# Kernel optimization log

Measured on AMD Instinct MI355X. Metric: run time of the kernel, lower is better.

## Reference

```python
import jax, jax.numpy as jnp
import numpy as np

B, S, NB = 8, 512, 23
INIT, E, R, T = 512, 256, 3, 2
NEG = -9e8

def _gru(x, h, wih, whh, bih, bhh):
    gi = x @ wih.T + bih
    gh = h @ whh.T + bhh
    ir, iz, inn = jnp.split(gi, 3, axis=-1)
    hr, hz, hn = jnp.split(gh, 3, axis=-1)
    r = jax.nn.sigmoid(ir + hr)
    z = jax.nn.sigmoid(iz + hz)
    n = jnp.tanh(inn + r * hn)
    return (1.0 - z) * n + z * h

def setup_inputs():
    key = jax.random.key(0)
    ks = jax.random.split(key, 30)
    def lin(k, o, i):
        return jax.random.normal(k, (o, i), jnp.float32) * 0.02
    def vec(k, n):
        return jax.random.normal(k, (n,), jnp.float32) * 0.02
    inp = {}
    inp["amino_list"] = jax.random.normal(ks[0], (B, S, INIT), jnp.float32)
    inp["amino_mask"] = (jax.random.uniform(ks[1], (B, S)) < 0.9).astype(jnp.float32)
    inp["emb_W"] = lin(ks[2], E, INIT); inp["emb_b"] = vec(ks[3], E)
    inp["nb_W"] = lin(ks[4], E, INIT); inp["nb_b"] = vec(ks[5], E)
    inp["align_W"] = jax.random.normal(ks[6], (R, 1, 2 * E), jnp.float32) * 0.02
    inp["align_b"] = jax.random.normal(ks[7], (R, 1), jnp.float32) * 0.02
    inp["attend_W"] = jax.random.normal(ks[8], (R, E, E), jnp.float32) * 0.02
    inp["attend_b"] = jax.random.normal(ks[9], (R, E), jnp.float32) * 0.02
    inp["gru_wih"] = jax.random.normal(ks[10], (R, 3 * E, E), jnp.float32) * 0.02
    inp["gru_whh"] = jax.random.normal(ks[11], (R, 3 * E, E), jnp.float32) * 0.02
    inp["gru_bih"] = jax.random.normal(ks[12], (R, 3 * E), jnp.float32) * 0.02
    inp["gru_bhh"] = jax.random.normal(ks[13], (R, 3 * E), jnp.float32) * 0.02
    inp["seq_align_W"] = lin(ks[14], 1, 2 * E); inp["seq_align_b"] = vec(ks[15], 1)
    inp["seq_attend_W"] = lin(ks[16], E, E); inp["seq_attend_b"] = vec(ks[17], E)
    inp["seq_gru_wih"] = lin(ks[18], 3 * E, E); inp["seq_gru_bih"] = vec(ks[19], 3 * E)
    inp["seq_gru_whh"] = lin(ks[20], 3 * E, E); inp["seq_gru_bhh"] = vec(ks[21], 3 * E)
    inp["amino_degree_list"] = jax.random.randint(ks[22], (B, S, NB), -1, S)
    return inp

def reference(amino_list, amino_mask, emb_W, emb_b, nb_W, nb_b, align_W, align_b,
              attend_W, attend_b, gru_wih, gru_whh, gru_bih, gru_bhh,
              seq_align_W, seq_align_b, seq_attend_W, seq_attend_b,
              seq_gru_wih, seq_gru_whh, seq_gru_bih, seq_gru_bhh, amino_degree_list):
    idx = amino_degree_list
    lrelu = jax.nn.leaky_relu
    # per-batch neighbor gather: (S,D),(S,NB) -> (S,NB,D); index -1 wraps (masked out below)
    gather = jax.vmap(lambda f, i: f[i])
    feat = lrelu(amino_list @ emb_W.T + emb_b)               # (B,S,E)
    nfeat = lrelu(gather(amino_list, idx) @ nb_W.T + nb_b)   # (B,S,NB,E)
    attend_mask = (idx != -1).astype(feat.dtype)             # (B,S,NB)
    smask = jnp.where(idx == -1, NEG, 0.0).astype(feat.dtype)

    def attn(d, center, nbr):
        # align Linear on concat([center, nbr]) split into two matvecs (same math, no concat)
        aW = align_W[d, 0]
        score = lrelu(jnp.einsum('bse,e->bs', center, aW[:E])[:, :, None]
                      + jnp.einsum('bsne,e->bsn', nbr, aW[E:]) + align_b[d, 0])
        w = jax.nn.softmax(score + smask, axis=-1) * attend_mask   # softmax over neighbor axis
        nt = nbr @ attend_W[d].T + attend_b[d]
        return jax.nn.elu(jnp.einsum('bsn,bsne->bse', w, nt))

    h = _gru(attn(0, feat, nfeat).reshape(-1, E), feat.reshape(-1, E),
             gru_wih[0], gru_whh[0], gru_bih[0], gru_bhh[0])
    act = jax.nn.relu(h.reshape(B, S, E))
    for d in range(1, R):
        ctx = attn(d, act, gather(act, idx))
        h = _gru(ctx.reshape(-1, E), h, gru_wih[d], gru_whh[d], gru_bih[d], gru_bhh[d])
        act = jax.nn.relu(h.reshape(B, S, E))

    seq_feature = jnp.sum(act * amino_mask[:, :, None], axis=1)  # (B,E)
    act_mol = jax.nn.relu(seq_feature)                           # fixed across T (as in torch)
    seq_smask = jnp.where(amino_mask == 0, NEG, 0.0)
    saW = seq_align_W[0]
    act_seq = act_mol
    for _ in range(T):
        score = lrelu((act_mol @ saW[:E])[:, None]
                      + jnp.einsum('bse,e->bs', act, saW[E:]) + seq_align_b[0])
        w = jax.nn.softmax(score + seq_smask, axis=-1) * amino_mask  # softmax over seq axis
        tf = act @ seq_attend_W.T + seq_attend_b
        seq_ctx = jax.nn.elu(jnp.einsum('bs,bse->be', w, tf))
        seq_feature = _gru(seq_ctx, seq_feature, seq_gru_wih, seq_gru_whh, seq_gru_bih, seq_gru_bhh)
        act_seq = jax.nn.relu(seq_feature)
    return (act_seq, act)
```

## Files before the change

### kernel.cpp

```cpp
#include <hip/hip_runtime.h>
#include <math.h>


#define BSZ   8
#define SEQ   512
#define NBR   23
#define EMB   256
#define INITD 512
#define BS    (BSZ*SEQ)
#define G3    (3*EMB)
#define NEGV  -9e8f

typedef __attribute__((ext_vector_type(8))) short short8;
typedef __attribute__((ext_vector_type(4))) float f32x4;

__device__ __forceinline__ float lrelu(float x){ return x > 0.f ? x : 0.01f*x; }
__device__ __forceinline__ float elu1 (float x){ return x > 0.f ? x : (expf(x)-1.f); }
__device__ __forceinline__ float sigm (float x){ return 1.f/(1.f+expf(-x)); }
__device__ __forceinline__ float bf2f(ushort u){
    union { unsigned int i; float f; } v; v.i = ((unsigned int)u) << 16; return v.f;
}
__device__ __forceinline__ ushort f2bf(float f){
    union { float f; unsigned int i; } v; v.f = f;
    unsigned int u = v.i;
    return (ushort)((u + 0x7FFFu + ((u >> 16) & 1u)) >> 16);
}
__device__ __forceinline__ unsigned pk2(float a, float b){
    return (unsigned)f2bf(a) | ((unsigned)f2bf(b) << 16);
}
__device__ __forceinline__ void unpack8(uint4 v, float* o) {
    o[0]=bf2f((ushort)(v.x&0xffff)); o[1]=bf2f((ushort)(v.x>>16));
    o[2]=bf2f((ushort)(v.y&0xffff)); o[3]=bf2f((ushort)(v.y>>16));
    o[4]=bf2f((ushort)(v.z&0xffff)); o[5]=bf2f((ushort)(v.z>>16));
    o[6]=bf2f((ushort)(v.w&0xffff)); o[7]=bf2f((ushort)(v.w>>16));
}

__device__ __forceinline__ void gload_lds16(const void* g, void* l) {
    __builtin_amdgcn_global_load_lds(
        (const __attribute__((address_space(1))) unsigned int*)g,
        (__attribute__((address_space(3))) unsigned int*)l,
        16, 0, 0);
}

__global__ __launch_bounds__(256) void convert9_kernel(
    const float* s0, ushort* d0, int n0,
    const float* s1, ushort* d1, int n1,
    const float* s2, ushort* d2, int n2,
    const float* s3, ushort* d3, int n3,
    const float* s4, ushort* d4, int n4,
    const float* s5, ushort* d5, int n5,
    const float* s6, ushort* d6, int n6,
    const float* s7, ushort* d7, int n7,
    const float* s8, ushort* d8, int n8)
{
    const float* srcs[9] = {s0,s1,s2,s3,s4,s5,s6,s7,s8};
    ushort* dsts[9] = {d0,d1,d2,d3,d4,d5,d6,d7,d8};
    int ns[9] = {n0,n1,n2,n3,n4,n5,n6,n7,n8};
    int seg = blockIdx.y;
    const float* s = srcs[seg]; ushort* d = dsts[seg]; int n = ns[seg];
    size_t i = ((size_t)blockIdx.x * 256 + threadIdx.x) * 8;
    size_t stride = (size_t)gridDim.x * 256 * 8;
    for (; i < (size_t)n; i += stride) {
        float4 a = *reinterpret_cast<const float4*>(s + i);
        float4 b = *reinterpret_cast<const float4*>(s + i + 4);
        uint4 o;
        o.x = pk2(a.x, a.y); o.y = pk2(a.z, a.w);
        o.z = pk2(b.x, b.y); o.w = pk2(b.z, b.w);
        *reinterpret_cast<uint4*>(d + i) = o;
    }
}

struct GemmLds64 { ushort A[2][128][64]; ushort B[2][64][64]; };

template<int ACT>
__device__ __forceinline__ void gemm64_dev(
    const ushort* __restrict__ A, const ushort* __restrict__ W,
    const float* __restrict__ bias,
    float* __restrict__ C, ushort* __restrict__ Cbf,
    int N, int K, int bx, int by, GemmLds64& L)
{
    const int tid = threadIdx.x;
    const int m0 = bx * 128, n0 = by * 64;
    const int wv = tid >> 6, lane = tid & 63;
    const int fr = lane & 15, grp = lane >> 4;
    const int kc = K >> 3;
    const int mh = wv & 1, nh = wv >> 1;
    const int lrow = lane >> 3;
    const int csrc = (lane & 7) ^ lrow;

    f32x4 acc[4][2];
    #pragma unroll
    for (int i = 0; i < 4; ++i)
        #pragma unroll
        for (int n = 0; n < 2; ++n) acc[i][n] = (f32x4){0.f,0.f,0.f,0.f};

    auto stage = [&](int c, int k0) {
        const int kch = (k0 >> 3) + csrc;
        #pragma unroll
        for (int i = 0; i < 4; ++i) {
            const int s = (wv << 2) + i;
            gload_lds16(A + ((size_t)(m0 + (s << 3) + lrow) * kc + kch) * 8,
                        &L.A[c][s << 3][0]);
        }
        #pragma unroll
        for (int i = 0; i < 2; ++i) {
            const int s = (wv << 1) + i;
            gload_lds16(W + ((size_t)(n0 + (s << 3) + lrow) * kc + kch) * 8,
                        &L.B[c][s << 3][0]);
        }
    };
    auto compute = [&](int c) {
        #pragma unroll
        for (int ks = 0; ks < 2; ++ks) {
            short8 af[4];
            #pragma unroll
            for (int i = 0; i < 4; ++i) {
                const int ar = (mh << 6) + (i << 4) + fr;
                af[i] = *reinterpret_cast<const short8*>(
                    &L.A[c][ar][(((ks << 2) + grp) ^ (ar & 7)) << 3]);
            }
            #pragma unroll
            for (int n = 0; n < 2; ++n) {
                const int br = (nh << 5) + (n << 4) + fr;
                short8 bv = *reinterpret_cast<const short8*>(
                    &L.B[c][br][(((ks << 2) + grp) ^ (br & 7)) << 3]);
                #pragma unroll
                for (int i = 0; i < 4; ++i)
                    acc[i][n] = __builtin_amdgcn_mfma_f32_16x16x32_bf16(
                        af[i], bv, acc[i][n], 0, 0, 0);
            }
        }
    };

    const int KT = K >> 6;
    stage(0, 0);
    __syncthreads();
    int cur = 0;
    for (int kt = 1; kt < KT; ++kt) {
        stage(cur ^ 1, kt << 6);
        compute(cur);
        __syncthreads();
        cur ^= 1;
    }
    compute(cur);

    #pragma unroll
    for (int i = 0; i < 4; ++i) {
        const int mrow = m0 + (mh << 6) + (i << 4) + (grp << 2);
        #pragma unroll
        for (int n = 0; n < 2; ++n) {
            const int col = n0 + (nh << 5) + (n << 4) + fr;
            const float bv = bias[col];
            #pragma unroll
            for (int j = 0; j < 4; ++j) {
                float t = acc[i][n][j] + bv;
                if (ACT == 1) t = lrelu(t);
                size_t off = (size_t)(mrow + j) * N + col;
                if (C)   C[off] = t;
                if (Cbf) Cbf[off] = f2bf(t);
            }
        }
    }
}

__global__ __launch_bounds__(256) void featnbase_kernel(
    const ushort* __restrict__ aminobf,
    const ushort* __restrict__ embWbf, const float* __restrict__ embB,
    float* __restrict__ feat, ushort* __restrict__ featbf,
    const ushort* __restrict__ nbWbf, const float* __restrict__ nbB,
    float* __restrict__ nbase, ushort* __restrict__ nbasebf)
{
    __shared__ GemmLds64 L;
    int blk = blockIdx.x;
    if (blk < 128)
        gemm64_dev<1>(aminobf, embWbf, embB, feat, featbf, EMB, INITD, blk & 31, blk >> 5, L);
    else {
        blk -= 128;
        gemm64_dev<1>(aminobf, nbWbf, nbB, nbase, nbasebf, EMB, INITD, blk & 31, blk >> 5, L);
    }
}

__global__ __launch_bounds__(256) void dot2_kernel(
    const float* __restrict__ center, const float* __restrict__ nbrbase,
    const float* __restrict__ alignWd,
    float* __restrict__ cdot, float* __restrict__ ndot)
{
    const int lane = threadIdx.x & 63;
    const int wv   = threadIdx.x >> 6;
    const int e    = lane << 2;
    const int rb   = blockIdx.x * 32 + wv * 8;
    float4 w0 = *reinterpret_cast<const float4*>(&alignWd[e]);
    float4 w1 = *reinterpret_cast<const float4*>(&alignWd[EMB + e]);
    #pragma unroll
    for (int i = 0; i < 8; ++i) {
        const int r = rb + i;
        float4 xc = *reinterpret_cast<const float4*>(&center[(size_t)r*EMB + e]);
        float4 xn = *reinterpret_cast<const float4*>(&nbrbase[(size_t)r*EMB + e]);
        float ac = xc.x*w0.x + xc.y*w0.y + xc.z*w0.z + xc.w*w0.w;
        float an = xn.x*w1.x + xn.y*w1.y + xn.z*w1.z + xn.w*w1.w;
        #pragma unroll
        for (int off = 32; off; off >>= 1) {
            ac += __shfl_xor(ac, off, 64);
            an += __shfl_xor(an, off, 64);
        }
        if (lane == 0) { cdot[r] = ac; ndot[r] = an; }
    }
}

struct GALds { ushort ctxpre[16][256]; ushort ctx[16][256]; float wsum_s[16]; };

__global__ __launch_bounds__(512) void gatherattend_kernel(
    const float* __restrict__ cdot, const float* __restrict__ ndot,
    const int* __restrict__ idx, const ushort* __restrict__ nbr,
    const float* __restrict__ alignBd,
    const ushort* __restrict__ attWd, const float* __restrict__ attBd,
    ushort* __restrict__ ctxbf)
{
    __shared__ GALds L;
    const int tid = threadIdx.x;
    const int r0 = blockIdx.x * 16;

    {
        const int row16 = tid >> 5, sub = tid & 31;
        const int r = r0 + row16, b = r >> 9;
        float sc = -3e38f, vm = 0.f; int rn = 0;
        if (sub < NBR) {
            int j = idx[(size_t)r*NBR + sub];
            int valid = (j >= 0);
            int jj = valid ? j : j + SEQ;
            rn = b*SEQ + jj;
            vm = (float)valid;
            sc = lrelu(cdot[r] + ndot[rn] + alignBd[0]) + (valid ? 0.f : NEGV);
        }
        float m = sc;
        #pragma unroll
        for (int off = 16; off; off >>= 1) m = fmaxf(m, __shfl_xor(m, off, 32));
        float ev = (sub < NBR) ? expf(sc - m) : 0.f;
        float s = ev;
        #pragma unroll
        for (int off = 16; off; off >>= 1) s += __shfl_xor(s, off, 32);
        float wgt = ev * vm / s;
        float ws = wgt;
        #pragma unroll
        for (int off = 16; off; off >>= 1) ws += __shfl_xor(ws, off, 32);
        float a8[8] = {};
        const int e0 = sub << 3;
        #pragma unroll
        for (int n = 0; n < NBR; ++n) {
            float wn = __shfl(wgt, n, 32);
            int   rr = __shfl(rn, n, 32);
            uint4 v = *reinterpret_cast<const uint4*>(&nbr[(size_t)rr*EMB + e0]);
            float x[8]; unpack8(v, x);
            #pragma unroll
            for (int i = 0; i < 8; ++i) a8[i] += wn * x[i];
        }
        uint4 o;
        o.x = pk2(a8[0],a8[1]); o.y = pk2(a8[2],a8[3]);
        o.z = pk2(a8[4],a8[5]); o.w = pk2(a8[6],a8[7]);
        *reinterpret_cast<uint4*>(&L.ctxpre[row16][(sub ^ (row16&7)) << 3]) = o;
        if (sub == 0) L.wsum_s[row16] = ws;
    }
    __syncthreads();

    const int wv = tid >> 6, lane = tid & 63;
    const int fr = lane & 15, grp = lane >> 4;
    {
        f32x4 acc[2] = {(f32x4){0,0,0,0},(f32x4){0,0,0,0}};
        #pragma unroll
        for (int kt = 0; kt < 8; ++kt) {
            short8 af = *reinterpret_cast<const short8*>(
                &L.ctxpre[fr][((((kt<<2)+grp) ^ (fr&7)) << 3)]);
            #pragma unroll
            for (int f = 0; f < 2; ++f) {
                const int col = (wv<<5) + (f<<4) + fr;
                short8 bv = *reinterpret_cast<const short8*>(
                    &attWd[(size_t)col*EMB + (kt<<5) + (grp<<3)]);
                acc[f] = __builtin_amdgcn_mfma_f32_16x16x32_bf16(af, bv, acc[f], 0, 0, 0);
            }
        }
        #pragma unroll
        for (int f = 0; f < 2; ++f) {
            const int col = (wv<<5) + (f<<4) + fr;
            const float bb = attBd[col];
            #pragma unroll
            for (int j = 0; j < 4; ++j) {
                const int row = (grp<<2) + j;
                L.ctx[row][col] = f2bf(elu1(acc[f][j] + L.wsum_s[row]*bb));
            }
        }
    }
    __syncthreads();
    {
        const int row = tid >> 5, c = tid & 31;
        uint4 v = *reinterpret_cast<const uint4*>(&L.ctx[row][c << 3]);
        *reinterpret_cast<uint4*>(&ctxbf[(size_t)(r0+row)*EMB + (c << 3)]) = v;
    }
}

__global__ __launch_bounds__(256) void gigh_kernel(
    const ushort* __restrict__ ctxbf, const ushort* __restrict__ gwihd,
    const float* __restrict__ gbihd, ushort* __restrict__ gibf,
    const ushort* __restrict__ hprevbf, const ushort* __restrict__ gwhhd,
    const float* __restrict__ gbhhd, ushort* __restrict__ ghbf)
{
    __shared__ GemmLds64 L;
    int blk = blockIdx.x;
    if (blk < 384)
        gemm64_dev<0>(ctxbf, gwihd, gbihd, nullptr, gibf, G3, EMB, blk & 31, blk >> 5, L);
    else {
        blk -= 384;
        gemm64_dev<0>(hprevbf, gwhhd, gbhhd, nullptr, ghbf, G3, EMB, blk & 31, blk >> 5, L);
    }
}

template<int LAST>
__global__ __launch_bounds__(512) void grudot_kernel(
    const ushort* __restrict__ gibf, const ushort* __restrict__ ghbf,
    const float* __restrict__ hprev, const float* __restrict__ nextW,
    float* __restrict__ hout, ushort* __restrict__ hbf,
    float* __restrict__ actout, ushort* __restrict__ actbf,
    float* __restrict__ cdotO, float* __restrict__ ndotO)
{
    const int tid = threadIdx.x;
    const int row = tid >> 5, sub = tid & 31;
    const int e0 = sub << 3;
    const size_t r = (size_t)blockIdx.x * 16 + row;
    const size_t gb = r*G3;
    uint4 giA = *reinterpret_cast<const uint4*>(&gibf[gb + e0]);
    uint4 giB = *reinterpret_cast<const uint4*>(&gibf[gb + 256 + e0]);
    uint4 giC = *reinterpret_cast<const uint4*>(&gibf[gb + 512 + e0]);
    uint4 ghA = *reinterpret_cast<const uint4*>(&ghbf[gb + e0]);
    uint4 ghB = *reinterpret_cast<const uint4*>(&ghbf[gb + 256 + e0]);
    uint4 ghC = *reinterpret_cast<const uint4*>(&ghbf[gb + 512 + e0]);
    float4 hp0 = *reinterpret_cast<const float4*>(&hprev[r*EMB + e0]);
    float4 hp1 = *reinterpret_cast<const float4*>(&hprev[r*EMB + e0 + 4]);
    float ir_[8], iz_[8], in_[8], hr_[8], hz_[8], hn_[8];
    unpack8(giA, ir_); unpack8(giB, iz_); unpack8(giC, in_);
    unpack8(ghA, hr_); unpack8(ghB, hz_); unpack8(ghC, hn_);
    const float hp_[8] = {hp0.x,hp0.y,hp0.z,hp0.w,hp1.x,hp1.y,hp1.z,hp1.w};
    float hv8[8], av8[8];
    #pragma unroll
    for (int i = 0; i < 8; ++i) {
        float rg = sigm(ir_[i] + hr_[i]);
        float z  = sigm(iz_[i] + hz_[i]);
        float n  = tanhf(in_[i] + rg*hn_[i]);
        hv8[i] = (1.f - z)*n + z*hp_[i];
        av8[i] = fmaxf(hv8[i], 0.f);
    }
    *reinterpret_cast<float4*>(&hout[r*EMB + e0])       = make_float4(hv8[0],hv8[1],hv8[2],hv8[3]);
    *reinterpret_cast<float4*>(&hout[r*EMB + e0 + 4])   = make_float4(hv8[4],hv8[5],hv8[6],hv8[7]);
    *reinterpret_cast<float4*>(&actout[r*EMB + e0])     = make_float4(av8[0],av8[1],av8[2],av8[3]);
    *reinterpret_cast<float4*>(&actout[r*EMB + e0 + 4]) = make_float4(av8[4],av8[5],av8[6],av8[7]);
    uint4 hb, ab;
    hb.x = pk2(hv8[0],hv8[1]); hb.y = pk2(hv8[2],hv8[3]);
    hb.z = pk2(hv8[4],hv8[5]); hb.w = pk2(hv8[6],hv8[7]);
    ab.x = pk2(av8[0],av8[1]); ab.y = pk2(av8[2],av8[3]);
    ab.z = pk2(av8[4],av8[5]); ab.w = pk2(av8[6],av8[7]);
    *reinterpret_cast<uint4*>(&hbf[r*EMB + e0])   = hb;
    *reinterpret_cast<uint4*>(&actbf[r*EMB + e0]) = ab;
    float pc = 0.f, pn = 0.f;
    float4 w1a = *reinterpret_cast<const float4*>(&nextW[EMB + e0]);
    float4 w1b = *reinterpret_cast<const float4*>(&nextW[EMB + e0 + 4]);
    pn = av8[0]*w1a.x + av8[1]*w1a.y + av8[2]*w1a.z + av8[3]*w1a.w
       + av8[4]*w1b.x + av8[5]*w1b.y + av8[6]*w1b.z + av8[7]*w1b.w;
    if (!LAST) {
        float4 w0a = *reinterpret_cast<const float4*>(&nextW[e0]);
        float4 w0b = *reinterpret_cast<const float4*>(&nextW[e0 + 4]);
        pc = av8[0]*w0a.x + av8[1]*w0a.y + av8[2]*w0a.z + av8[3]*w0a.w
           + av8[4]*w0b.x + av8[5]*w0b.y + av8[6]*w0b.z + av8[7]*w0b.w;
    }
    #pragma unroll
    for (int off = 16; off; off >>= 1) {
        pn += __shfl_xor(pn, off, 32);
        if (!LAST) pc += __shfl_xor(pc, off, 32);
    }
    if (sub == 0) {
        if (!LAST) cdotO[r] = pc;
        ndotO[r] = pn;
    }
}

__global__ __launch_bounds__(256) void seqpre_kernel(
    const ushort* __restrict__ actbf, const ushort* __restrict__ satWbf,
    const float* __restrict__ satB, float* __restrict__ tf,
    const float* __restrict__ act, const float* __restrict__ mask,
    const float* __restrict__ saW,
    float* __restrict__ seqfeat, float* __restrict__ cmol)
{
    __shared__ GemmLds64 L;
    int blk = blockIdx.x;
    if (blk < 128) {
        gemm64_dev<0>(actbf, satWbf, satB, tf, nullptr, EMB, EMB, blk & 31, blk >> 5, L);
    } else {
        const int b = blk - 128;
        const int e = threadIdx.x;
        float acc = 0.f;
        for (int s = 0; s < SEQ; ++s)
            acc += act[((size_t)b*SEQ + s)*EMB + e] * mask[b*SEQ + s];
        seqfeat[b*EMB + e] = acc;
        float* red = reinterpret_cast<float*>(&L);
        red[e] = fmaxf(acc, 0.f) * saW[e];
        __syncthreads();
        for (int off = 128; off; off >>= 1) {
            if (e < off) red[e] += red[e + off];
            __syncthreads();
        }
        if (e == 0) cmol[b] = red[0];
    }
}

__global__ __launch_bounds__(256) void seqpv2_kernel(
    const float* __restrict__ ad, const float* __restrict__ mask,
    const float* __restrict__ saB, const float* __restrict__ cmol,
    const float* __restrict__ tf, float* __restrict__ partial)
{
    const int st = blockIdx.x, b = blockIdx.y;
    const int tid = threadIdx.x;
    __shared__ float w_s[SEQ];
    __shared__ float red[256];
    float mk0 = mask[b*SEQ + tid], mk1 = mask[b*SEQ + 256 + tid];
    float cb = cmol[b], bb = saB[0];
    float s0 = lrelu(cb + ad[b*SEQ + tid] + bb)       + (mk0 == 0.f ? NEGV : 0.f);
    float s1 = lrelu(cb + ad[b*SEQ + 256 + tid] + bb) + (mk1 == 0.f ? NEGV : 0.f);
    red[tid] = fmaxf(s0, s1); __syncthreads();
    for (int off = 128; off; off >>= 1) {
        if (tid < off) red[tid] = fmaxf(red[tid], red[tid + off]);
        __syncthreads();
    }
    float m = red[0]; __syncthreads();
    float e0 = expf(s0 - m), e1 = expf(s1 - m);
    red[tid] = e0 + e1; __syncthreads();
    for (int off = 128; off; off >>= 1) {
        if (tid < off) red[tid] += red[tid + off];
        __syncthreads();
    }
    float inv = 1.f / red[0];
    w_s[tid]       = e0 * inv * mk0;
    w_s[tid + 256] = e1 * inv * mk1;
    __syncthreads();
    float acc = 0.f;
    const int s0i = st * 32;
    #pragma unroll 4
    for (int s = s0i; s < s0i + 32; ++s)
        acc += w_s[s] * tf[((size_t)b*SEQ + s)*EMB + tid];
    partial[((size_t)b*16 + st)*EMB + tid] = acc;
}

template<int T0>
__global__ __launch_bounds__(512) void seqstep_kernel(
    const float* __restrict__ partial, const float* __restrict__ sfin,
    const ushort* __restrict__ sgwihbf, const float* __restrict__ sgbih,
    const ushort* __restrict__ sgwhhbf, const float* __restrict__ sgbhh,
    float* __restrict__ sgi, float* __restrict__ sfout,
    float* __restrict__ actseq)
{
    const int b = blockIdx.x >> 2, q = blockIdx.x & 3;
    const int tid = threadIdx.x, lane = tid & 63, wv = tid >> 6;
    __shared__ float xs[EMB];
    __shared__ float hs[EMB];
    __shared__ float gis[192], ghs[192];
    if (tid < EMB) {
        hs[tid] = sfin[b*EMB + tid];
        if (T0) {
            float a = 0.f;
            #pragma unroll
            for (int st = 0; st < 16; ++st)
                a += partial[((size_t)b*16 + st)*EMB + tid];
            xs[tid] = elu1(a);
        }
    }
    if (!T0) {
        for (int l = tid; l < 192; l += 512) {
            int g = (l >> 6)*EMB + (q << 6) + (l & 63);
            gis[l] = sgi[b*G3 + g];
        }
    }
    __syncthreads();
    const int nrows = T0 ? 384 : 192;
    const int rpw = nrows >> 3;
    for (int i = 0; i < rpw; ++i) {
        const int l = wv * rpw + i;
        const int iswih = T0 && (l < 192);
        const int ll = (T0 && l >= 192) ? l - 192 : l;
        const int g = (ll >> 6)*EMB + (q << 6) + (ll & 63);
        const ushort* Wm = iswih ? sgwihbf : sgwhhbf;
        ushort4 w4 = *reinterpret_cast<const ushort4*>(&Wm[(size_t)g*EMB + (lane << 2)]);
        float4 x4 = *reinterpret_cast<const float4*>(iswih ? &xs[lane << 2] : &hs[lane << 2]);
        float d = bf2f(w4.x)*x4.x + bf2f(w4.y)*x4.y + bf2f(w4.z)*x4.z + bf2f(w4.w)*x4.w;
        #pragma unroll
        for (int off = 32; off; off >>= 1) d += __shfl_xor(d, off, 64);
        if (lane == 0) {
            if (iswih) {
                d += sgbih[g];
                gis[ll] = d;
                sgi[b*G3 + g] = d;
            } else {
                ghs[ll] = d + sgbhh[g];
            }
        }
    }
    __syncthreads();
    if (tid < 64) {
        const int e = (q << 6) + tid;
        float rg = sigm(gis[tid]       + ghs[tid]);
        float z  = sigm(gis[64 + tid]  + ghs[64 + tid]);
        float n  = tanhf(gis[128 + tid] + rg*ghs[128 + tid]);
        float hv = (1.f - z)*n + z*hs[e];
        sfout[b*EMB + e]  = hv;
        actseq[b*EMB + e] = fmaxf(hv, 0.f);
    }
}

extern "C" void kernel_launch(void* const* d_in, const int* in_sizes, int n_in,
                              void* d_out, int out_size, void* d_ws, size_t ws_size,
                              hipStream_t stream) {
    (void)in_sizes; (void)n_in; (void)out_size; (void)ws_size;
    const float* amino  = (const float*)d_in[0];
    const float* mask   = (const float*)d_in[1];
    const float* embW   = (const float*)d_in[2];
    const float* embB   = (const float*)d_in[3];
    const float* nbW    = (const float*)d_in[4];
    const float* nbB    = (const float*)d_in[5];
    const float* alignW = (const float*)d_in[6];
    const float* alignB = (const float*)d_in[7];
    const float* attW   = (const float*)d_in[8];
    const float* attB   = (const float*)d_in[9];
    const float* gwih   = (const float*)d_in[10];
    const float* gwhh   = (const float*)d_in[11];
    const float* gbih   = (const float*)d_in[12];
    const float* gbhh   = (const float*)d_in[13];
    const float* saW    = (const float*)d_in[14];
    const float* saB    = (const float*)d_in[15];
    const float* satW   = (const float*)d_in[16];
    const float* satB   = (const float*)d_in[17];
    const float* sgwih  = (const float*)d_in[18];
    const float* sgbih  = (const float*)d_in[19];
    const float* sgwhh  = (const float*)d_in[20];
    const float* sgbhh  = (const float*)d_in[21];
    const int*   idx    = (const int*)d_in[22];

    char* cur = (char*)d_ws;
    auto alloc = [&](size_t bytes) -> char* {
        char* p = cur; cur += (bytes + 255) & ~(size_t)255; return p;
    };
    float* feat    = (float*)alloc((size_t)BS*EMB*4);
    float* nbase   = (float*)alloc((size_t)BS*EMB*4);
    float* h       = (float*)alloc((size_t)BS*EMB*4);
    float* tf      = (float*)alloc((size_t)BS*EMB*4);
    float* cdot    = (float*)alloc(BS*4);
    float* ndot    = (float*)alloc(BS*4);
    float* seqfeat = (float*)alloc(BSZ*EMB*4);
    float* sf2     = (float*)alloc(BSZ*EMB*4);
    float* cmol    = (float*)alloc(64*4);
    float* sgi     = (float*)alloc(BSZ*G3*4);
    float* partial = (float*)alloc((size_t)BSZ*16*EMB*4);
    ushort* aminobf  = (ushort*)alloc((size_t)BS*INITD*2);
    ushort* featbf   = (ushort*)alloc((size_t)BS*EMB*2);
    ushort* nbasebf  = (ushort*)alloc((size_t)BS*EMB*2);
    ushort* actbf    = (ushort*)alloc((size_t)BS*EMB*2);
    ushort* hbf      = (ushort*)alloc((size_t)BS*EMB*2);
    ushort* ctxbf    = (ushort*)alloc((size_t)BS*EMB*2);
    ushort* gibf     = (ushort*)alloc((size_t)BS*G3*2);
    ushort* ghbf     = (ushort*)alloc((size_t)BS*G3*2);
    ushort* embWbf   = (ushort*)alloc((size_t)EMB*INITD*2);
    ushort* nbWbf    = (ushort*)alloc((size_t)EMB*INITD*2);
    ushort* attWbf   = (ushort*)alloc((size_t)3*EMB*EMB*2);
    ushort* gwihbf   = (ushort*)alloc((size_t)3*G3*EMB*2);
    ushort* gwhhbf   = (ushort*)alloc((size_t)3*G3*EMB*2);
    ushort* satWbf   = (ushort*)alloc((size_t)EMB*EMB*2);
    ushort* sgwihbf  = (ushort*)alloc((size_t)G3*EMB*2);
    ushort* sgwhhbf  = (ushort*)alloc((size_t)G3*EMB*2);

    float* out    = (float*)d_out;
    float* actseq = out;
    float* act    = out + BSZ*EMB;

    convert9_kernel<<<dim3(1024, 9), 256, 0, stream>>>(
        amino, aminobf, BS*INITD,
        embW,  embWbf,  EMB*INITD,
        nbW,   nbWbf,   EMB*INITD,
        attW,  attWbf,  3*EMB*EMB,
        gwih,  gwihbf,  3*G3*EMB,
        gwhh,  gwhhbf,  3*G3*EMB,
        satW,  satWbf,  EMB*EMB,
        sgwih, sgwihbf, G3*EMB,
        sgwhh, sgwhhbf, G3*EMB);

    featnbase_kernel<<<256, 256, 0, stream>>>(
        aminobf, embWbf, embB, feat, featbf, nbWbf, nbB, nbase, nbasebf);

    dot2_kernel<<<128, 256, 0, stream>>>(feat, nbase, alignW, cdot, ndot);

    for (int d = 0; d < 3; ++d) {
        const ushort* nbrbf   = (d == 0) ? nbasebf : actbf;
        const float*  hprev   = (d == 0) ? feat    : h;
        const ushort* hprevbf = (d == 0) ? featbf  : hbf;
        gatherattend_kernel<<<BS/16, 512, 0, stream>>>(
            cdot, ndot, idx, nbrbf, alignB + d,
            attWbf + (size_t)d*EMB*EMB, attB + d*EMB, ctxbf);
        gigh_kernel<<<768, 256, 0, stream>>>(
            ctxbf, gwihbf + (size_t)d*G3*EMB, gbih + d*G3, gibf,
            hprevbf, gwhhbf + (size_t)d*G3*EMB, gbhh + d*G3, ghbf);
        if (d < 2) {
            grudot_kernel<0><<<BS/16, 512, 0, stream>>>(
                gibf, ghbf, hprev, alignW + (d+1)*2*EMB,
                h, hbf, act, actbf, cdot, ndot);
        } else {
            grudot_kernel<1><<<BS/16, 512, 0, stream>>>(
                gibf, ghbf, hprev, saW,
                h, hbf, act, actbf, cdot, ndot);
        }
    }

    seqpre_kernel<<<136, 256, 0, stream>>>(
        actbf, satWbf, satB, tf, act, mask, saW, seqfeat, cmol);
    seqpv2_kernel<<<dim3(16, BSZ), 256, 0, stream>>>(ndot, mask, saB, cmol, tf, partial);
    seqstep_kernel<1><<<32, 512, 0, stream>>>(
        partial, seqfeat, sgwihbf, sgbih, sgwhhbf, sgbhh, sgi, sf2, actseq);
    seqstep_kernel<0><<<32, 512, 0, stream>>>(
        partial, sf2, sgwihbf, sgbih, sgwhhbf, sgbhh, sgi, seqfeat, actseq);
}
```

Measured before the change: 186.6 us.

## Fuse sequence pooling into GRU epilogue and merge sequence readout kernels

Replaces the per-segment convert kernel with a flat grid-stride converter that also zeroes the pooled sequence-feature buffer. The last GRU epilogue now does the masked sum over sequence positions in shared memory and atomically adds into seqfeat, so the serial per-batch loop in seqpre is removed. The softmax, weighted pooling and first GRU step are merged into one kernel, and a lighter second-step kernel computes only the hidden-state GEMV. The fp32 h buffer is dropped in favour of reading the bf16 copy of the previous hidden state, which adds rounding error, and the atomic pooling makes the summation order nondeterministic.

```diff
diff --git a/kernel.cpp b/kernel.cpp
--- a/kernel.cpp
+++ b/kernel.cpp
@@ -42,25 +42,37 @@
         16, 0, 0);
 }
 
-__global__ __launch_bounds__(256) void convert9_kernel(
-    const float* s0, ushort* d0, int n0,
-    const float* s1, ushort* d1, int n1,
-    const float* s2, ushort* d2, int n2,
-    const float* s3, ushort* d3, int n3,
-    const float* s4, ushort* d4, int n4,
-    const float* s5, ushort* d5, int n5,
-    const float* s6, ushort* d6, int n6,
-    const float* s7, ushort* d7, int n7,
-    const float* s8, ushort* d8, int n8)
-{
-    const float* srcs[9] = {s0,s1,s2,s3,s4,s5,s6,s7,s8};
-    ushort* dsts[9] = {d0,d1,d2,d3,d4,d5,d6,d7,d8};
-    int ns[9] = {n0,n1,n2,n3,n4,n5,n6,n7,n8};
-    int seg = blockIdx.y;
-    const float* s = srcs[seg]; ushort* d = dsts[seg]; int n = ns[seg];
-    size_t i = ((size_t)blockIdx.x * 256 + threadIdx.x) * 8;
-    size_t stride = (size_t)gridDim.x * 256 * 8;
-    for (; i < (size_t)n; i += stride) {
+__global__ __launch_bounds__(256) void convert_flat(
+    const float* __restrict__ amino, ushort* __restrict__ aminobf,
+    const float* __restrict__ embW,  ushort* __restrict__ embWbf,
+    const float* __restrict__ nbW,   ushort* __restrict__ nbWbf,
+    const float* __restrict__ attW,  ushort* __restrict__ attWbf,
+    const float* __restrict__ gwih,  ushort* __restrict__ gwihbf,
+    const float* __restrict__ gwhh,  ushort* __restrict__ gwhhbf,
+    const float* __restrict__ satW,  ushort* __restrict__ satWbf,
+    const float* __restrict__ sgwih, ushort* __restrict__ sgwihbf,
+    const float* __restrict__ sgwhh, ushort* __restrict__ sgwhhbf,
+    float* __restrict__ seqfeatZ)
+{
+    const unsigned stride = gridDim.x * 256;
+    for (unsigned u = blockIdx.x*256 + threadIdx.x; u < 524544u; u += stride) {
+        const float* s; ushort* d; unsigned lu;
+        if      (u < 262144u) { s=amino; d=aminobf; lu=u; }
+        else if (u < 278528u) { s=embW;  d=embWbf;  lu=u-262144u; }
+        else if (u < 294912u) { s=nbW;   d=nbWbf;   lu=u-278528u; }
+        else if (u < 319488u) { s=attW;  d=attWbf;  lu=u-294912u; }
+        else if (u < 393216u) { s=gwih;  d=gwihbf;  lu=u-319488u; }
+        else if (u < 466944u) { s=gwhh;  d=gwhhbf;  lu=u-393216u; }
+        else if (u < 475136u) { s=satW;  d=satWbf;  lu=u-466944u; }
+        else if (u < 499712u) { s=sgwih; d=sgwihbf; lu=u-475136u; }
+        else if (u < 524288u) { s=sgwhh; d=sgwhhbf; lu=u-499712u; }
+        else {
+            unsigned i = (u - 524288u) * 8;
+            *reinterpret_cast<float4*>(&seqfeatZ[i])     = make_float4(0,0,0,0);
+            *reinterpret_cast<float4*>(&seqfeatZ[i + 4]) = make_float4(0,0,0,0);
+            continue;
+        }
+        size_t i = (size_t)lu * 8;
         float4 a = *reinterpret_cast<const float4*>(s + i);
         float4 b = *reinterpret_cast<const float4*>(s + i + 4);
         uint4 o;
@@ -316,11 +328,14 @@
 template<int LAST>
 __global__ __launch_bounds__(512) void grudot_kernel(
     const ushort* __restrict__ gibf, const ushort* __restrict__ ghbf,
-    const float* __restrict__ hprev, const float* __restrict__ nextW,
-    float* __restrict__ hout, ushort* __restrict__ hbf,
-    float* __restrict__ actout, ushort* __restrict__ actbf,
-    float* __restrict__ cdotO, float* __restrict__ ndotO)
-{
+    const ushort* __restrict__ hprevbf, const float* __restrict__ nextW,
+    const float* __restrict__ mask,
+    ushort* __restrict__ hbf, float* __restrict__ actout,
+    ushort* __restrict__ actbf,
+    float* __restrict__ cdotO, float* __restrict__ ndotO,
+    float* __restrict__ seqfeatA)
+{
+    __shared__ float sred[16][256];
     const int tid = threadIdx.x;
     const int row = tid >> 5, sub = tid & 31;
     const int e0 = sub << 3;
@@ -332,12 +347,11 @@
     uint4 ghA = *reinterpret_cast<const uint4*>(&ghbf[gb + e0]);
     uint4 ghB = *reinterpret_cast<const uint4*>(&ghbf[gb + 256 + e0]);
     uint4 ghC = *reinterpret_cast<const uint4*>(&ghbf[gb + 512 + e0]);
-    float4 hp0 = *reinterpret_cast<const float4*>(&hprev[r*EMB + e0]);
-    float4 hp1 = *reinterpret_cast<const float4*>(&hprev[r*EMB + e0 + 4]);
-    float ir_[8], iz_[8], in_[8], hr_[8], hz_[8], hn_[8];
+    uint4 hpv = *reinterpret_cast<const uint4*>(&hprevbf[r*EMB + e0]);
+    float ir_[8], iz_[8], in_[8], hr_[8], hz_[8], hn_[8], hp_[8];
     unpack8(giA, ir_); unpack8(giB, iz_); unpack8(giC, in_);
     unpack8(ghA, hr_); unpack8(ghB, hz_); unpack8(ghC, hn_);
-    const float hp_[8] = {hp0.x,hp0.y,hp0.z,hp0.w,hp1.x,hp1.y,hp1.z,hp1.w};
+    unpack8(hpv, hp_);
     float hv8[8], av8[8];
     #pragma unroll
     for (int i = 0; i < 8; ++i) {
@@ -347,10 +361,10 @@
         hv8[i] = (1.f - z)*n + z*hp_[i];
         av8[i] = fmaxf(hv8[i], 0.f);
     }
-    *reinterpret_cast<float4*>(&hout[r*EMB + e0])       = make_float4(hv8[0],hv8[1],hv8[2],hv8[3]);
-    *reinterpret_cast<float4*>(&hout[r*EMB + e0 + 4])   = make_float4(hv8[4],hv8[5],hv8[6],hv8[7]);
-    *reinterpret_cast<float4*>(&actout[r*EMB + e0])     = make_float4(av8[0],av8[1],av8[2],av8[3]);
-    *reinterpret_cast<float4*>(&actout[r*EMB + e0 + 4]) = make_float4(av8[4],av8[5],av8[6],av8[7]);
+    if (LAST) {
+        *reinterpret_cast<float4*>(&actout[r*EMB + e0])     = make_float4(av8[0],av8[1],av8[2],av8[3]);
+        *reinterpret_cast<float4*>(&actout[r*EMB + e0 + 4]) = make_float4(av8[4],av8[5],av8[6],av8[7]);
+    }
     uint4 hb, ab;
     hb.x = pk2(hv8[0],hv8[1]); hb.y = pk2(hv8[2],hv8[3]);
     hb.z = pk2(hv8[4],hv8[5]); hb.w = pk2(hv8[6],hv8[7]);
@@ -378,77 +392,33 @@
         if (!LAST) cdotO[r] = pc;
         ndotO[r] = pn;
     }
+    if (LAST) {
+        const float mk = mask[r];
+        #pragma unroll
+        for (int i = 0; i < 8; ++i) sred[row][e0 + i] = av8[i] * mk;
+        __syncthreads();
+        if (tid < 256) {
+            float s = 0.f;
+            #pragma unroll
+            for (int rr = 0; rr < 16; ++rr) s += sred[rr][tid];
+            atomicAdd(&seqfeatA[(blockIdx.x >> 5)*EMB + tid], s);
+        }
+    }
 }
 
 __global__ __launch_bounds__(256) void seqpre_kernel(
     const ushort* __restrict__ actbf, const ushort* __restrict__ satWbf,
-    const float* __restrict__ satB, float* __restrict__ tf,
-    const float* __restrict__ act, const float* __restrict__ mask,
-    const float* __restrict__ saW,
-    float* __restrict__ seqfeat, float* __restrict__ cmol)
+    const float* __restrict__ satB, float* __restrict__ tf)
 {
     __shared__ GemmLds64 L;
-    int blk = blockIdx.x;
-    if (blk < 128) {
-        gemm64_dev<0>(actbf, satWbf, satB, tf, nullptr, EMB, EMB, blk & 31, blk >> 5, L);
-    } else {
-        const int b = blk - 128;
-        const int e = threadIdx.x;
-        float acc = 0.f;
-        for (int s = 0; s < SEQ; ++s)
-            acc += act[((size_t)b*SEQ + s)*EMB + e] * mask[b*SEQ + s];
-        seqfeat[b*EMB + e] = acc;
-        float* red = reinterpret_cast<float*>(&L);
-        red[e] = fmaxf(acc, 0.f) * saW[e];
-        __syncthreads();
-        for (int off = 128; off; off >>= 1) {
-            if (e < off) red[e] += red[e + off];
-            __syncthreads();
-        }
-        if (e == 0) cmol[b] = red[0];
-    }
-}
-
-__global__ __launch_bounds__(256) void seqpv2_kernel(
+    gemm64_dev<0>(actbf, satWbf, satB, tf, nullptr, EMB, EMB,
+                  blockIdx.x & 31, blockIdx.x >> 5, L);
+}
+
+__global__ __launch_bounds__(512) void seqstep0_kernel(
     const float* __restrict__ ad, const float* __restrict__ mask,
-    const float* __restrict__ saB, const float* __restrict__ cmol,
-    const float* __restrict__ tf, float* __restrict__ partial)
-{
-    const int st = blockIdx.x, b = blockIdx.y;
-    const int tid = threadIdx.x;
-    __shared__ float w_s[SEQ];
-    __shared__ float red[256];
-    float mk0 = mask[b*SEQ + tid], mk1 = mask[b*SEQ + 256 + tid];
-    float cb = cmol[b], bb = saB[0];
-    float s0 = lrelu(cb + ad[b*SEQ + tid] + bb)       + (mk0 == 0.f ? NEGV : 0.f);
-    float s1 = lrelu(cb + ad[b*SEQ + 256 + tid] + bb) + (mk1 == 0.f ? NEGV : 0.f);
-    red[tid] = fmaxf(s0, s1); __syncthreads();
-    for (int off = 128; off; off >>= 1) {
-        if (tid < off) red[tid] = fmaxf(red[tid], red[tid + off]);
-        __syncthreads();
-    }
-    float m = red[0]; __syncthreads();
-    float e0 = expf(s0 - m), e1 = expf(s1 - m);
-    red[tid] = e0 + e1; __syncthreads();
-    for (int off = 128; off; off >>= 1) {
-        if (tid < off) red[tid] += red[tid + off];
-        __syncthreads();
-    }
-    float inv = 1.f / red[0];
-    w_s[tid]       = e0 * inv * mk0;
-    w_s[tid + 256] = e1 * inv * mk1;
-    __syncthreads();
-    float acc = 0.f;
-    const int s0i = st * 32;
-    #pragma unroll 4
-    for (int s = s0i; s < s0i + 32; ++s)
-        acc += w_s[s] * tf[((size_t)b*SEQ + s)*EMB + tid];
-    partial[((size_t)b*16 + st)*EMB + tid] = acc;
-}
-
-template<int T0>
-__global__ __launch_bounds__(512) void seqstep_kernel(
-    const float* __restrict__ partial, const float* __restrict__ sfin,
+    const float* __restrict__ saB, const float* __restrict__ saW,
+    const float* __restrict__ seqfeat, const float* __restrict__ tf,
     const ushort* __restrict__ sgwihbf, const float* __restrict__ sgbih,
     const ushort* __restrict__ sgwhhbf, const float* __restrict__ sgbhh,
     float* __restrict__ sgi, float* __restrict__ sfout,
@@ -456,32 +426,52 @@
 {
     const int b = blockIdx.x >> 2, q = blockIdx.x & 3;
     const int tid = threadIdx.x, lane = tid & 63, wv = tid >> 6;
-    __shared__ float xs[EMB];
-    __shared__ float hs[EMB];
-    __shared__ float gis[192], ghs[192];
+    __shared__ float xs[EMB], hs[EMB], gis[192], ghs[192];
+    __shared__ float w_s[SEQ], red[SEQ], pv[2][EMB];
     if (tid < EMB) {
-        hs[tid] = sfin[b*EMB + tid];
-        if (T0) {
-            float a = 0.f;
-            #pragma unroll
-            for (int st = 0; st < 16; ++st)
-                a += partial[((size_t)b*16 + st)*EMB + tid];
-            xs[tid] = elu1(a);
-        }
-    }
-    if (!T0) {
-        for (int l = tid; l < 192; l += 512) {
-            int g = (l >> 6)*EMB + (q << 6) + (l & 63);
-            gis[l] = sgi[b*G3 + g];
-        }
-    }
-    __syncthreads();
-    const int nrows = T0 ? 384 : 192;
-    const int rpw = nrows >> 3;
-    for (int i = 0; i < rpw; ++i) {
-        const int l = wv * rpw + i;
-        const int iswih = T0 && (l < 192);
-        const int ll = (T0 && l >= 192) ? l - 192 : l;
+        float sf = seqfeat[b*EMB + tid];
+        hs[tid] = sf;
+        red[tid] = fmaxf(sf, 0.f) * saW[tid];
+    }
+    __syncthreads();
+    for (int off = 128; off; off >>= 1) {
+        if (tid < off) red[tid] += red[tid + off];
+        __syncthreads();
+    }
+    const float cmol = red[0];
+    __syncthreads();
+    const float mk = mask[b*SEQ + tid];
+    const float sc = lrelu(cmol + ad[b*SEQ + tid] + saB[0]) + (mk == 0.f ? NEGV : 0.f);
+    red[tid] = sc; __syncthreads();
+    for (int off = 256; off; off >>= 1) {
+        if (tid < off) red[tid] = fmaxf(red[tid], red[tid + off]);
+        __syncthreads();
+    }
+    const float m = red[0]; __syncthreads();
+    const float ev = expf(sc - m);
+    red[tid] = ev; __syncthreads();
+    for (int off = 256; off; off >>= 1) {
+        if (tid < off) red[tid] += red[tid + off];
+        __syncthreads();
+    }
+    w_s[tid] = ev / red[0] * mk;
+    __syncthreads();
+    {
+        const int e = tid & 255, scn = tid >> 8;
+        const float* tfb = &tf[((size_t)b*SEQ + scn*256)*EMB + e];
+        float acc = 0.f;
+        #pragma unroll 4
+        for (int s = 0; s < 256; ++s)
+            acc += w_s[scn*256 + s] * tfb[(size_t)s*EMB];
+        pv[scn][e] = acc;
+    }
+    __syncthreads();
+    if (tid < EMB) xs[tid] = elu1(pv[0][tid] + pv[1][tid]);
+    __syncthreads();
+    for (int i = 0; i < 48; ++i) {
+        const int l = wv * 48 + i;
+        const int iswih = (l < 192);
+        const int ll = iswih ? l : l - 192;
         const int g = (ll >> 6)*EMB + (q << 6) + (ll & 63);
         const ushort* Wm = iswih ? sgwihbf : sgwhhbf;
         ushort4 w4 = *reinterpret_cast<const ushort4*>(&Wm[(size_t)g*EMB + (lane << 2)]);
@@ -498,6 +488,44 @@
                 ghs[ll] = d + sgbhh[g];
             }
         }
+    }
+    __syncthreads();
+    if (tid < 64) {
+        const int e = (q << 6) + tid;
+        float rg = sigm(gis[tid]       + ghs[tid]);
+        float z  = sigm(gis[64 + tid]  + ghs[64 + tid]);
+        float n  = tanhf(gis[128 + tid] + rg*ghs[128 + tid]);
+        float hv = (1.f - z)*n + z*hs[e];
+        sfout[b*EMB + e]  = hv;
+        actseq[b*EMB + e] = fmaxf(hv, 0.f);
+    }
+}
+
+__global__ __launch_bounds__(512) void seqstep1_kernel(
+    const float* __restrict__ sfin,
+    const ushort* __restrict__ sgwhhbf, const float* __restrict__ sgbhh,
+    const float* __restrict__ sgi, float* __restrict__ sfout,
+    float* __restrict__ actseq)
+{
+    const int b = blockIdx.x >> 2, q = blockIdx.x & 3;
+    const int tid = threadIdx.x, lane = tid & 63, wv = tid >> 6;
+    __shared__ float hs[EMB];
+    __shared__ float gis[192], ghs[192];
+    if (tid < EMB) hs[tid] = sfin[b*EMB + tid];
+    for (int l = tid; l < 192; l += 512) {
+        int g = (l >> 6)*EMB + (q << 6) + (l & 63);
+        gis[l] = sgi[b*G3 + g];
+    }
+    __syncthreads();
+    for (int i = 0; i < 24; ++i) {
+        const int l = wv * 24 + i;
+        const int g = (l >> 6)*EMB + (q << 6) + (l & 63);
+        ushort4 w4 = *reinterpret_cast<const ushort4*>(&sgwhhbf[(size_t)g*EMB + (lane << 2)]);
+        float4 h4 = *reinterpret_cast<const float4*>(&hs[lane << 2]);
+        float d = bf2f(w4.x)*h4.x + bf2f(w4.y)*h4.y + bf2f(w4.z)*h4.z + bf2f(w4.w)*h4.w;
+        #pragma unroll
+        for (int off = 32; off; off >>= 1) d += __shfl_xor(d, off, 64);
+        if (lane == 0) ghs[l] = d + sgbhh[g];
     }
     __syncthreads();
     if (tid < 64) {
@@ -545,15 +573,12 @@
     };
     float* feat    = (float*)alloc((size_t)BS*EMB*4);
     float* nbase   = (float*)alloc((size_t)BS*EMB*4);
-    float* h       = (float*)alloc((size_t)BS*EMB*4);
     float* tf      = (float*)alloc((size_t)BS*EMB*4);
     float* cdot    = (float*)alloc(BS*4);
     float* ndot    = (float*)alloc(BS*4);
     float* seqfeat = (float*)alloc(BSZ*EMB*4);
     float* sf2     = (float*)alloc(BSZ*EMB*4);
-    float* cmol    = (float*)alloc(64*4);
     float* sgi     = (float*)alloc(BSZ*G3*4);
-    float* partial = (float*)alloc((size_t)BSZ*16*EMB*4);
     ushort* aminobf  = (ushort*)alloc((size_t)BS*INITD*2);
     ushort* featbf   = (ushort*)alloc((size_t)BS*EMB*2);
     ushort* nbasebf  = (ushort*)alloc((size_t)BS*EMB*2);
@@ -575,16 +600,10 @@
     float* actseq = out;
     float* act    = out + BSZ*EMB;
 
-    convert9_kernel<<<dim3(1024, 9), 256, 0, stream>>>(
-        amino, aminobf, BS*INITD,
-        embW,  embWbf,  EMB*INITD,
-        nbW,   nbWbf,   EMB*INITD,
-        attW,  attWbf,  3*EMB*EMB,
-        gwih,  gwihbf,  3*G3*EMB,
-        gwhh,  gwhhbf,  3*G3*EMB,
-        satW,  satWbf,  EMB*EMB,
-        sgwih, sgwihbf, G3*EMB,
-        sgwhh, sgwhhbf, G3*EMB);
+    convert_flat<<<2048, 256, 0, stream>>>(
+        amino, aminobf, embW, embWbf, nbW, nbWbf, attW, attWbf,
+        gwih, gwihbf, gwhh, gwhhbf, satW, satWbf,
+        sgwih, sgwihbf, sgwhh, sgwhhbf, seqfeat);
 
     featnbase_kernel<<<256, 256, 0, stream>>>(
         aminobf, embWbf, embB, feat, featbf, nbWbf, nbB, nbase, nbasebf);
@@ -593,7 +612,6 @@
 
     for (int d = 0; d < 3; ++d) {
         const ushort* nbrbf   = (d == 0) ? nbasebf : actbf;
-        const float*  hprev   = (d == 0) ? feat    : h;
         const ushort* hprevbf = (d == 0) ? featbf  : hbf;
         gatherattend_kernel<<<BS/16, 512, 0, stream>>>(
             cdot, ndot, idx, nbrbf, alignB + d,
@@ -603,20 +621,19 @@
             hprevbf, gwhhbf + (size_t)d*G3*EMB, gbhh + d*G3, ghbf);
         if (d < 2) {
             grudot_kernel<0><<<BS/16, 512, 0, stream>>>(
-                gibf, ghbf, hprev, alignW + (d+1)*2*EMB,
-                h, hbf, act, actbf, cdot, ndot);
+                gibf, ghbf, hprevbf, alignW + (d+1)*2*EMB, mask,
+                hbf, act, actbf, cdot, ndot, seqfeat);
         } else {
             grudot_kernel<1><<<BS/16, 512, 0, stream>>>(
-                gibf, ghbf, hprev, saW,
-                h, hbf, act, actbf, cdot, ndot);
-        }
-    }
-
-    seqpre_kernel<<<136, 256, 0, stream>>>(
-        actbf, satWbf, satB, tf, act, mask, saW, seqfeat, cmol);
-    seqpv2_kernel<<<dim3(16, BSZ), 256, 0, stream>>>(ndot, mask, saB, cmol, tf, partial);
-    seqstep_kernel<1><<<32, 512, 0, stream>>>(
-        partial, seqfeat, sgwihbf, sgbih, sgwhhbf, sgbhh, sgi, sf2, actseq);
-    seqstep_kernel<0><<<32, 512, 0, stream>>>(
-        partial, sf2, sgwihbf, sgbih, sgwhhbf, sgbhh, sgi, seqfeat, actseq);
-}
+                gibf, ghbf, hprevbf, saW, mask,
+                hbf, act, actbf, cdot, ndot, seqfeat);
+        }
+    }
+
+    seqpre_kernel<<<128, 256, 0, stream>>>(actbf, satWbf, satB, tf);
+    seqstep0_kernel<<<32, 512, 0, stream>>>(
+        ndot, mask, saB, saW, seqfeat, tf,
+        sgwihbf, sgbih, sgwhhbf, sgbhh, sgi, sf2, actseq);
+    seqstep1_kernel<<<32, 512, 0, stream>>>(
+        sf2, sgwhhbf, sgbhh, sgi, seqfeat, actseq);
+}
```

Result: faster. 177.0 us (-5.1%).
